# Performance work log

Measured on AMD Instinct MI355X. Metric: run time of the kernel, lower is better.

The kernel has to match this reference:

```python
import jax, jax.numpy as jnp
import numpy as np

BITS = 4
GROUPSIZE = 128
IN_FEATURES = 4096
OUT_FEATURES = 11008
PACK = 32 // BITS  # 8 nibbles per int32
MASK = (1 << BITS) - 1


def setup_inputs() -> dict:
    key = jax.random.key(0)
    k1, k2, k3, k4, k5 = jax.random.split(key, 5)
    x = jax.random.normal(k1, (4, 2048, IN_FEATURES), dtype=jnp.float32)
    qweight = jax.random.randint(k2, (IN_FEATURES // 32 * BITS, OUT_FEATURES), 0, 2147483647, dtype=jnp.int32)
    n_groups = IN_FEATURES // GROUPSIZE  # 32
    qzeros = jax.random.randint(k3, (n_groups, OUT_FEATURES // 32 * BITS), 0, 2147483647, dtype=jnp.int32)
    scales = jax.random.uniform(k4, (n_groups, OUT_FEATURES), dtype=jnp.float32) * 0.01 + 1e-3
    bias = jax.random.normal(k5, (OUT_FEATURES,), dtype=jnp.float32)
    return {"x": x, "qweight": qweight, "qzeros": qzeros, "scales": scales, "bias": bias}


def _dequant(qweight, qzeros, scales):
    # GPTQ 4-bit unpack + group-wise dequant (g_idx=None / non-act-order path).
    shifts = jnp.arange(0, 32, BITS, dtype=jnp.int32)  # [8]
    # zero points: (G, out//8) int32 -> (G, out)
    z = ((qzeros[:, :, None] >> shifts[None, None, :]) & MASK)
    z = z.reshape(qzeros.shape[0], -1).astype(scales.dtype)  # (G, out)
    # weights: (in//8, out) int32 -> (in//8, 8, out) -> (G, groupsize, out)
    w = ((qweight[:, None, :] >> shifts[None, :, None]) & MASK).astype(scales.dtype)
    n_groups = scales.shape[0]
    w = w.reshape(n_groups, GROUPSIZE, -1)
    # W = scale * q - scale * zero, per group
    W = scales[:, None, :] * w - (z * scales)[:, None, :]
    return W.reshape(IN_FEATURES, OUT_FEATURES)


def reference(x, qweight, qzeros, scales, bias):
    W = _dequant(qweight, qzeros, scales)  # (in, out) fp32
    return jnp.matmul(x, W) + bias
```

## Files before the change

### kernel.cpp

```cpp
#include <hip/hip_runtime.h>
#include <hip/hip_bf16.h>
#include <stdint.h>

#define M_DIM 8192
#define K_DIM 4096
#define N_DIM 11008

typedef int i32x4 __attribute__((ext_vector_type(4)));
typedef float f32x4 __attribute__((ext_vector_type(4)));

typedef __attribute__((address_space(1))) const void global_cvoid;
typedef __attribute__((address_space(3))) void lds_void;

__device__ __forceinline__ void gload_lds16(const void* g, void* l) {
  __builtin_amdgcn_global_load_lds((global_cvoid*)g, (lds_void*)l, 16, 0, 0);
}

__global__ void k_quant_x(const float* __restrict__ x, signed char* __restrict__ xq,
                          float* __restrict__ sx) {
  int m = blockIdx.x;
  int tx = threadIdx.x;
  const float4* row = (const float4*)(x + (size_t)m * K_DIM);
  float4 v[4];
  float mx = 0.f;
  #pragma unroll
  for (int i = 0; i < 4; ++i) {
    v[i] = row[tx * 4 + i];
    mx = fmaxf(mx, fmaxf(fmaxf(fabsf(v[i].x), fabsf(v[i].y)),
                         fmaxf(fabsf(v[i].z), fabsf(v[i].w))));
  }
  #pragma unroll
  for (int off = 1; off < 64; off <<= 1)
    mx = fmaxf(mx, __shfl_xor(mx, off));
  __shared__ float wmx[4];
  if ((tx & 63) == 0) wmx[tx >> 6] = mx;
  __syncthreads();
  mx = fmaxf(fmaxf(wmx[0], wmx[1]), fmaxf(wmx[2], wmx[3]));
  mx = fmaxf(mx, 1e-20f);
  float scale = 127.0f / mx;
  if (tx == 0) sx[m] = mx / 127.0f;
  union { signed char c[16]; uint4 u; } p;
  #pragma unroll
  for (int i = 0; i < 4; ++i) {
    p.c[i * 4 + 0] = (signed char)(int)rintf(v[i].x * scale);
    p.c[i * 4 + 1] = (signed char)(int)rintf(v[i].y * scale);
    p.c[i * 4 + 2] = (signed char)(int)rintf(v[i].z * scale);
    p.c[i * 4 + 3] = (signed char)(int)rintf(v[i].w * scale);
  }
  ((uint4*)(xq + (size_t)m * K_DIM))[tx] = p.u;
}

__global__ void k_dequant_w8(const int* __restrict__ qw, const int* __restrict__ qz,
                             signed char* __restrict__ wt) {
  int n = blockIdx.x * blockDim.x + threadIdx.x;
  int k8_0 = blockIdx.y * 8;
  int g = (k8_0 * 8) >> 7;
  int zq = (qz[g * (N_DIM / 8) + (n >> 3)] >> ((n & 7) * 4)) & 15;
  #pragma unroll
  for (int i = 0; i < 8; ++i) {
    int k8 = k8_0 + i;
    int w = qw[(size_t)k8 * N_DIM + n];
    union { signed char c[8]; uint2 u; } r;
    #pragma unroll
    for (int j = 0; j < 8; ++j)
      r.c[j] = (signed char)(((w >> (4 * j)) & 15) - zq);
    *(uint2*)(wt + (size_t)n * K_DIM + (size_t)k8 * 8) = r.u;
  }
}


#define MFMA16(ks) do { \
  __builtin_amdgcn_s_setprio(1); \
  acci[0][0] = __builtin_amdgcn_mfma_i32_16x16x64_i8(af[0], bf[0], acci[0][0], 0, 0, 0); \
  acci[0][1] = __builtin_amdgcn_mfma_i32_16x16x64_i8(af[0], bf[1], acci[0][1], 0, 0, 0); \
  acci[0][2] = __builtin_amdgcn_mfma_i32_16x16x64_i8(af[0], bf[2], acci[0][2], 0, 0, 0); \
  acci[0][3] = __builtin_amdgcn_mfma_i32_16x16x64_i8(af[0], bf[3], acci[0][3], 0, 0, 0); \
  acci[1][0] = __builtin_amdgcn_mfma_i32_16x16x64_i8(af[1], bf[0], acci[1][0], 0, 0, 0); \
  acci[1][1] = __builtin_amdgcn_mfma_i32_16x16x64_i8(af[1], bf[1], acci[1][1], 0, 0, 0); \
  acci[1][2] = __builtin_amdgcn_mfma_i32_16x16x64_i8(af[1], bf[2], acci[1][2], 0, 0, 0); \
  acci[1][3] = __builtin_amdgcn_mfma_i32_16x16x64_i8(af[1], bf[3], acci[1][3], 0, 0, 0); \
  acci[2][0] = __builtin_amdgcn_mfma_i32_16x16x64_i8(af[2], bf[0], acci[2][0], 0, 0, 0); \
  acci[2][1] = __builtin_amdgcn_mfma_i32_16x16x64_i8(af[2], bf[1], acci[2][1], 0, 0, 0); \
  acci[2][2] = __builtin_amdgcn_mfma_i32_16x16x64_i8(af[2], bf[2], acci[2][2], 0, 0, 0); \
  acci[2][3] = __builtin_amdgcn_mfma_i32_16x16x64_i8(af[2], bf[3], acci[2][3], 0, 0, 0); \
  acci[3][0] = __builtin_amdgcn_mfma_i32_16x16x64_i8(af[3], bf[0], acci[3][0], 0, 0, 0); \
  acci[3][1] = __builtin_amdgcn_mfma_i32_16x16x64_i8(af[3], bf[1], acci[3][1], 0, 0, 0); \
  acci[3][2] = __builtin_amdgcn_mfma_i32_16x16x64_i8(af[3], bf[2], acci[3][2], 0, 0, 0); \
  acci[3][3] = __builtin_amdgcn_mfma_i32_16x16x64_i8(af[3], bf[3], acci[3][3], 0, 0, 0); \
  __builtin_amdgcn_s_setprio(0); \
} while (0)

#define LOADF(buf, ks) do { \
  const unsigned char* base_ = sh + (buf) * 32768; \
  af[0] = *(const i32x4*)(const void*)(base_ + (aoff0 ^ ((ks) << 6))); \
  af[1] = *(const i32x4*)(const void*)(base_ + (aoff1 ^ ((ks) << 6))); \
  af[2] = *(const i32x4*)(const void*)(base_ + (aoff2 ^ ((ks) << 6))); \
  af[3] = *(const i32x4*)(const void*)(base_ + (aoff3 ^ ((ks) << 6))); \
  bf[0] = *(const i32x4*)(const void*)(base_ + 16384 + (boff0 ^ ((ks) << 6))); \
  bf[1] = *(const i32x4*)(const void*)(base_ + 16384 + (boff1 ^ ((ks) << 6))); \
  bf[2] = *(const i32x4*)(const void*)(base_ + 16384 + (boff2 ^ ((ks) << 6))); \
  bf[3] = *(const i32x4*)(const void*)(base_ + 16384 + (boff3 ^ ((ks) << 6))); \
} while (0)

#define STAGE_ALL(buf, kt) do { \
  unsigned char* la_ = sh + (buf) * 32768 + w * 4096; \
  unsigned char* lb_ = la_ + 16384; \
  gload_lds16(pA + (kt) * 128, la_); \
  gload_lds16(pA + 8 * (size_t)K_DIM + (kt) * 128, la_ + 1024); \
  gload_lds16(pA + 16 * (size_t)K_DIM + (kt) * 128, la_ + 2048); \
  gload_lds16(pA + 24 * (size_t)K_DIM + (kt) * 128, la_ + 3072); \
  gload_lds16(pB + (kt) * 128, lb_); \
  gload_lds16(pB + 8 * (size_t)K_DIM + (kt) * 128, lb_ + 1024); \
  gload_lds16(pB + 16 * (size_t)K_DIM + (kt) * 128, lb_ + 2048); \
  gload_lds16(pB + 24 * (size_t)K_DIM + (kt) * 128, lb_ + 3072); \
} while (0)

#define WAIT_VM0 asm volatile("s_waitcnt vmcnt(0)" ::: "memory")
#define BAR() do { __builtin_amdgcn_s_barrier(); asm volatile("" ::: "memory"); } while (0)

__global__ __launch_bounds__(256, 2) void k_gemm8(const signed char* __restrict__ xq,
                                                  const signed char* __restrict__ wq,
                                                  const float* __restrict__ sc,
                                                  const float* __restrict__ sx,
                                                  const float* __restrict__ bias,
                                                  float* __restrict__ out) {
  __shared__ __align__(16) unsigned char sh[2 * 32768];

  const int nwg = gridDim.x;
  int bid = blockIdx.x;
  int swz = (bid & 7) * (nwg >> 3) + (bid >> 3);
  const int ntn = N_DIM / 128;
  int mt = swz / ntn;
  int nt = swz % ntn;

  const int tid = threadIdx.x;
  const int w = tid >> 6;
  const int lane = tid & 63;
  const int wm = w >> 1;
  const int wn = w & 1;
  const int fr = lane & 15;
  const int fq = lane >> 4;
  const int r7 = fr & 7;

  const int srow = lane >> 3;
  const int sslot = (lane & 7) ^ srow;
  const size_t goff = (size_t)srow * K_DIM + (size_t)sslot * 16;
  const signed char* pA = xq + (size_t)(mt * 128 + w * 32) * K_DIM + goff;
  const signed char* pB = wq + (size_t)(nt * 128 + w * 32) * K_DIM + goff;

  const int swb = (fq ^ r7) << 4;
  const int aoff0 = (wm * 64 + 0 * 16 + fr) * 128 + swb;
  const int aoff1 = (wm * 64 + 1 * 16 + fr) * 128 + swb;
  const int aoff2 = (wm * 64 + 2 * 16 + fr) * 128 + swb;
  const int aoff3 = (wm * 64 + 3 * 16 + fr) * 128 + swb;
  const int boff0 = (wn * 64 + 0 * 16 + fr) * 128 + swb;
  const int boff1 = (wn * 64 + 1 * 16 + fr) * 128 + swb;
  const int boff2 = (wn * 64 + 2 * 16 + fr) * 128 + swb;
  const int boff3 = (wn * 64 + 3 * 16 + fr) * 128 + swb;

  const int c0 = nt * 128 + wn * 64 + fr;

  i32x4 acci[4][4] = {};
  f32x4 accf[4][4] = {};
  i32x4 af[4], bf[4];

  STAGE_ALL(0, 0);
  WAIT_VM0;
  BAR();

  for (int t = 0; t < 32; ++t) {
    int buf = t & 1;
    if (t < 31) STAGE_ALL(buf ^ 1, t + 1);
    float sg0 = sc[(size_t)t * N_DIM + c0 + 0];
    float sg1 = sc[(size_t)t * N_DIM + c0 + 16];
    float sg2 = sc[(size_t)t * N_DIM + c0 + 32];
    float sg3 = sc[(size_t)t * N_DIM + c0 + 48];
    LOADF(buf, 0);
    MFMA16(0);
    LOADF(buf, 1);
    MFMA16(1);
    #pragma unroll
    for (int mi = 0; mi < 4; ++mi) {
      #pragma unroll
      for (int r = 0; r < 4; ++r) {
        accf[mi][0][r] += sg0 * (float)acci[mi][0][r];
        accf[mi][1][r] += sg1 * (float)acci[mi][1][r];
        accf[mi][2][r] += sg2 * (float)acci[mi][2][r];
        accf[mi][3][r] += sg3 * (float)acci[mi][3][r];
      }
      acci[mi][0] = (i32x4)(0); acci[mi][1] = (i32x4)(0);
      acci[mi][2] = (i32x4)(0); acci[mi][3] = (i32x4)(0);
    }
    WAIT_VM0;
    BAR();
  }

  const int r0 = mt * 128 + wm * 64 + fq * 4;
  #pragma unroll
  for (int mi = 0; mi < 4; ++mi) {
    float sxr[4];
    #pragma unroll
    for (int r = 0; r < 4; ++r) sxr[r] = sx[r0 + mi * 16 + r];
    #pragma unroll
    for (int nj = 0; nj < 4; ++nj) {
      int col = c0 + nj * 16;
      float bv = bias[col];
      size_t base = (size_t)(r0 + mi * 16) * N_DIM + col;
      #pragma unroll
      for (int r = 0; r < 4; ++r)
        out[base + (size_t)r * N_DIM] = sxr[r] * accf[mi][nj][r] + bv;
    }
  }
}

__global__ void k_fallback(const float* __restrict__ x, const int* __restrict__ qw,
                           const int* __restrict__ qz, const float* __restrict__ sc,
                           const float* __restrict__ bias, float* __restrict__ out) {
  int n = blockIdx.x * blockDim.x + threadIdx.x;
  int m = blockIdx.y;
  const float* xr = x + (size_t)m * K_DIM;
  float acc = 0.f;
  for (int g = 0; g < 32; ++g) {
    float s = sc[g * N_DIM + n];
    int zq = (qz[g * (N_DIM / 8) + (n >> 3)] >> ((n & 7) * 4)) & 15;
    float zs = s * (float)zq;
    for (int k8 = g * 16; k8 < g * 16 + 16; ++k8) {
      int w = qw[(size_t)k8 * N_DIM + n];
      #pragma unroll
      for (int j = 0; j < 8; ++j) {
        float wf = s * (float)((w >> (4 * j)) & 15) - zs;
        acc += wf * xr[k8 * 8 + j];
      }
    }
  }
  out[(size_t)m * N_DIM + n] = acc + bias[n];
}

extern "C" void kernel_launch(void* const* d_in, const int* in_sizes, int n_in,
                              void* d_out, int out_size, void* d_ws, size_t ws_size,
                              hipStream_t stream) {
  const float* x  = (const float*)d_in[0];
  const int* qw   = (const int*)d_in[1];
  const int* qz   = (const int*)d_in[2];
  const float* sc = (const float*)d_in[3];
  const float* bias = (const float*)d_in[4];
  float* out = (float*)d_out;

  const size_t xq_bytes = (size_t)M_DIM * K_DIM;
  const size_t sx_bytes = (size_t)M_DIM * sizeof(float);
  const size_t wq_bytes = (size_t)N_DIM * K_DIM;
  const size_t need = xq_bytes + sx_bytes + wq_bytes;

  if (ws_size >= need) {
    signed char* xq = (signed char*)d_ws;
    float* sx = (float*)((char*)d_ws + xq_bytes);
    signed char* wq = (signed char*)((char*)d_ws + xq_bytes + sx_bytes);
    k_quant_x<<<dim3(M_DIM), dim3(256), 0, stream>>>(x, xq, sx);
    k_dequant_w8<<<dim3(N_DIM / 256, 64), dim3(256), 0, stream>>>(qw, qz, wq);
    k_gemm8<<<dim3((M_DIM / 128) * (N_DIM / 128)), dim3(256), 0, stream>>>(xq, wq, sc, sx, bias, out);
  } else {
    k_fallback<<<dim3(N_DIM / 256, M_DIM), dim3(256), 0, stream>>>(x, qw, qz, sc, bias, out);
  }
}
```

Before: 585.0 us.

## Load A fragments directly to registers, stage only B in LDS, merge prep kernels

The GEMM now reads the int8 activation fragments straight from global memory into registers, with a register double-buffer across K tiles, and stages only the weight tile through LDS. This halves LDS usage and LDS reads per tile. The MFMA chain now starts each tile from a zero accumulator, which removes the explicit zeroing. The activation-quantisation and weight-dequant kernels are merged into one launch to save a kernel boundary. The cost is more VGPR pressure and uncoalesced 16-byte global loads for A that no longer go through swizzled LDS.

```diff
diff --git a/kernel.cpp b/kernel.cpp
--- a/kernel.cpp
+++ b/kernel.cpp
@@ -16,107 +16,163 @@
   __builtin_amdgcn_global_load_lds((global_cvoid*)g, (lds_void*)l, 16, 0, 0);
 }
 
-__global__ void k_quant_x(const float* __restrict__ x, signed char* __restrict__ xq,
-                          float* __restrict__ sx) {
-  int m = blockIdx.x;
-  int tx = threadIdx.x;
-  const float4* row = (const float4*)(x + (size_t)m * K_DIM);
-  float4 v[4];
-  float mx = 0.f;
-  #pragma unroll
-  for (int i = 0; i < 4; ++i) {
-    v[i] = row[tx * 4 + i];
-    mx = fmaxf(mx, fmaxf(fmaxf(fabsf(v[i].x), fabsf(v[i].y)),
-                         fmaxf(fabsf(v[i].z), fabsf(v[i].w))));
-  }
-  #pragma unroll
-  for (int off = 1; off < 64; off <<= 1)
-    mx = fmaxf(mx, __shfl_xor(mx, off));
-  __shared__ float wmx[4];
-  if ((tx & 63) == 0) wmx[tx >> 6] = mx;
-  __syncthreads();
-  mx = fmaxf(fmaxf(wmx[0], wmx[1]), fmaxf(wmx[2], wmx[3]));
-  mx = fmaxf(mx, 1e-20f);
-  float scale = 127.0f / mx;
-  if (tx == 0) sx[m] = mx / 127.0f;
-  union { signed char c[16]; uint4 u; } p;
-  #pragma unroll
-  for (int i = 0; i < 4; ++i) {
-    p.c[i * 4 + 0] = (signed char)(int)rintf(v[i].x * scale);
-    p.c[i * 4 + 1] = (signed char)(int)rintf(v[i].y * scale);
-    p.c[i * 4 + 2] = (signed char)(int)rintf(v[i].z * scale);
-    p.c[i * 4 + 3] = (signed char)(int)rintf(v[i].w * scale);
-  }
-  ((uint4*)(xq + (size_t)m * K_DIM))[tx] = p.u;
-}
-
-__global__ void k_dequant_w8(const int* __restrict__ qw, const int* __restrict__ qz,
-                             signed char* __restrict__ wt) {
-  int n = blockIdx.x * blockDim.x + threadIdx.x;
-  int k8_0 = blockIdx.y * 8;
-  int g = (k8_0 * 8) >> 7;
-  int zq = (qz[g * (N_DIM / 8) + (n >> 3)] >> ((n & 7) * 4)) & 15;
-  #pragma unroll
-  for (int i = 0; i < 8; ++i) {
-    int k8 = k8_0 + i;
-    int w = qw[(size_t)k8 * N_DIM + n];
-    union { signed char c[8]; uint2 u; } r;
-    #pragma unroll
-    for (int j = 0; j < 8; ++j)
-      r.c[j] = (signed char)(((w >> (4 * j)) & 15) - zq);
-    *(uint2*)(wt + (size_t)n * K_DIM + (size_t)k8 * 8) = r.u;
-  }
-}
-
-
-#define MFMA16(ks) do { \
+__global__ void k_prep(const float* __restrict__ x, signed char* __restrict__ xq,
+                       float* __restrict__ sx, const int* __restrict__ qw,
+                       const int* __restrict__ qz, signed char* __restrict__ wt) {
+  if (blockIdx.x < M_DIM) {
+    int m = blockIdx.x;
+    int tx = threadIdx.x;
+    const float4* row = (const float4*)(x + (size_t)m * K_DIM);
+    float4 v[4];
+    float mx = 0.f;
+    #pragma unroll
+    for (int i = 0; i < 4; ++i) {
+      v[i] = row[tx * 4 + i];
+      mx = fmaxf(mx, fmaxf(fmaxf(fabsf(v[i].x), fabsf(v[i].y)),
+                           fmaxf(fabsf(v[i].z), fabsf(v[i].w))));
+    }
+    #pragma unroll
+    for (int off = 1; off < 64; off <<= 1)
+      mx = fmaxf(mx, __shfl_xor(mx, off));
+    __shared__ float wmx[4];
+    if ((tx & 63) == 0) wmx[tx >> 6] = mx;
+    __syncthreads();
+    mx = fmaxf(fmaxf(wmx[0], wmx[1]), fmaxf(wmx[2], wmx[3]));
+    mx = fmaxf(mx, 1e-20f);
+    float scale = 127.0f / mx;
+    if (tx == 0) sx[m] = mx / 127.0f;
+    union { signed char c[16]; uint4 u; } p;
+    #pragma unroll
+    for (int i = 0; i < 4; ++i) {
+      p.c[i * 4 + 0] = (signed char)(int)rintf(v[i].x * scale);
+      p.c[i * 4 + 1] = (signed char)(int)rintf(v[i].y * scale);
+      p.c[i * 4 + 2] = (signed char)(int)rintf(v[i].z * scale);
+      p.c[i * 4 + 3] = (signed char)(int)rintf(v[i].w * scale);
+    }
+    ((uint4*)(xq + (size_t)m * K_DIM))[tx] = p.u;
+  } else {
+    int b = blockIdx.x - M_DIM;
+    int n = (b % 43) * 256 + threadIdx.x;
+    int k8_0 = (b / 43) * 8;
+    int g = (k8_0 * 8) >> 7;
+    int zq = (qz[g * (N_DIM / 8) + (n >> 3)] >> ((n & 7) * 4)) & 15;
+    #pragma unroll
+    for (int i = 0; i < 8; ++i) {
+      int k8 = k8_0 + i;
+      int w = qw[(size_t)k8 * N_DIM + n];
+      union { signed char c[8]; uint2 u; } r;
+      #pragma unroll
+      for (int j = 0; j < 8; ++j)
+        r.c[j] = (signed char)(((w >> (4 * j)) & 15) - zq);
+      *(uint2*)(wt + (size_t)n * K_DIM + (size_t)k8 * 8) = r.u;
+    }
+  }
+}
+
+
+#define MFMA_FIRST(S) do { \
   __builtin_amdgcn_s_setprio(1); \
-  acci[0][0] = __builtin_amdgcn_mfma_i32_16x16x64_i8(af[0], bf[0], acci[0][0], 0, 0, 0); \
-  acci[0][1] = __builtin_amdgcn_mfma_i32_16x16x64_i8(af[0], bf[1], acci[0][1], 0, 0, 0); \
-  acci[0][2] = __builtin_amdgcn_mfma_i32_16x16x64_i8(af[0], bf[2], acci[0][2], 0, 0, 0); \
-  acci[0][3] = __builtin_amdgcn_mfma_i32_16x16x64_i8(af[0], bf[3], acci[0][3], 0, 0, 0); \
-  acci[1][0] = __builtin_amdgcn_mfma_i32_16x16x64_i8(af[1], bf[0], acci[1][0], 0, 0, 0); \
-  acci[1][1] = __builtin_amdgcn_mfma_i32_16x16x64_i8(af[1], bf[1], acci[1][1], 0, 0, 0); \
-  acci[1][2] = __builtin_amdgcn_mfma_i32_16x16x64_i8(af[1], bf[2], acci[1][2], 0, 0, 0); \
-  acci[1][3] = __builtin_amdgcn_mfma_i32_16x16x64_i8(af[1], bf[3], acci[1][3], 0, 0, 0); \
-  acci[2][0] = __builtin_amdgcn_mfma_i32_16x16x64_i8(af[2], bf[0], acci[2][0], 0, 0, 0); \
-  acci[2][1] = __builtin_amdgcn_mfma_i32_16x16x64_i8(af[2], bf[1], acci[2][1], 0, 0, 0); \
-  acci[2][2] = __builtin_amdgcn_mfma_i32_16x16x64_i8(af[2], bf[2], acci[2][2], 0, 0, 0); \
-  acci[2][3] = __builtin_amdgcn_mfma_i32_16x16x64_i8(af[2], bf[3], acci[2][3], 0, 0, 0); \
-  acci[3][0] = __builtin_amdgcn_mfma_i32_16x16x64_i8(af[3], bf[0], acci[3][0], 0, 0, 0); \
-  acci[3][1] = __builtin_amdgcn_mfma_i32_16x16x64_i8(af[3], bf[1], acci[3][1], 0, 0, 0); \
-  acci[3][2] = __builtin_amdgcn_mfma_i32_16x16x64_i8(af[3], bf[2], acci[3][2], 0, 0, 0); \
-  acci[3][3] = __builtin_amdgcn_mfma_i32_16x16x64_i8(af[3], bf[3], acci[3][3], 0, 0, 0); \
+  acci[0][0] = __builtin_amdgcn_mfma_i32_16x16x64_i8(S[0][0], bfr[0][0], zq4, 0, 0, 0); \
+  acci[0][1] = __builtin_amdgcn_mfma_i32_16x16x64_i8(S[0][0], bfr[1][0], zq4, 0, 0, 0); \
+  acci[0][2] = __builtin_amdgcn_mfma_i32_16x16x64_i8(S[0][0], bfr[2][0], zq4, 0, 0, 0); \
+  acci[0][3] = __builtin_amdgcn_mfma_i32_16x16x64_i8(S[0][0], bfr[3][0], zq4, 0, 0, 0); \
+  acci[1][0] = __builtin_amdgcn_mfma_i32_16x16x64_i8(S[1][0], bfr[0][0], zq4, 0, 0, 0); \
+  acci[1][1] = __builtin_amdgcn_mfma_i32_16x16x64_i8(S[1][0], bfr[1][0], zq4, 0, 0, 0); \
+  acci[1][2] = __builtin_amdgcn_mfma_i32_16x16x64_i8(S[1][0], bfr[2][0], zq4, 0, 0, 0); \
+  acci[1][3] = __builtin_amdgcn_mfma_i32_16x16x64_i8(S[1][0], bfr[3][0], zq4, 0, 0, 0); \
+  acci[2][0] = __builtin_amdgcn_mfma_i32_16x16x64_i8(S[2][0], bfr[0][0], zq4, 0, 0, 0); \
+  acci[2][1] = __builtin_amdgcn_mfma_i32_16x16x64_i8(S[2][0], bfr[1][0], zq4, 0, 0, 0); \
+  acci[2][2] = __builtin_amdgcn_mfma_i32_16x16x64_i8(S[2][0], bfr[2][0], zq4, 0, 0, 0); \
+  acci[2][3] = __builtin_amdgcn_mfma_i32_16x16x64_i8(S[2][0], bfr[3][0], zq4, 0, 0, 0); \
+  acci[3][0] = __builtin_amdgcn_mfma_i32_16x16x64_i8(S[3][0], bfr[0][0], zq4, 0, 0, 0); \
+  acci[3][1] = __builtin_amdgcn_mfma_i32_16x16x64_i8(S[3][0], bfr[1][0], zq4, 0, 0, 0); \
+  acci[3][2] = __builtin_amdgcn_mfma_i32_16x16x64_i8(S[3][0], bfr[2][0], zq4, 0, 0, 0); \
+  acci[3][3] = __builtin_amdgcn_mfma_i32_16x16x64_i8(S[3][0], bfr[3][0], zq4, 0, 0, 0); \
   __builtin_amdgcn_s_setprio(0); \
 } while (0)
 
-#define LOADF(buf, ks) do { \
-  const unsigned char* base_ = sh + (buf) * 32768; \
-  af[0] = *(const i32x4*)(const void*)(base_ + (aoff0 ^ ((ks) << 6))); \
-  af[1] = *(const i32x4*)(const void*)(base_ + (aoff1 ^ ((ks) << 6))); \
-  af[2] = *(const i32x4*)(const void*)(base_ + (aoff2 ^ ((ks) << 6))); \
-  af[3] = *(const i32x4*)(const void*)(base_ + (aoff3 ^ ((ks) << 6))); \
-  bf[0] = *(const i32x4*)(const void*)(base_ + 16384 + (boff0 ^ ((ks) << 6))); \
-  bf[1] = *(const i32x4*)(const void*)(base_ + 16384 + (boff1 ^ ((ks) << 6))); \
-  bf[2] = *(const i32x4*)(const void*)(base_ + 16384 + (boff2 ^ ((ks) << 6))); \
-  bf[3] = *(const i32x4*)(const void*)(base_ + 16384 + (boff3 ^ ((ks) << 6))); \
-} while (0)
-
-#define STAGE_ALL(buf, kt) do { \
-  unsigned char* la_ = sh + (buf) * 32768 + w * 4096; \
-  unsigned char* lb_ = la_ + 16384; \
-  gload_lds16(pA + (kt) * 128, la_); \
-  gload_lds16(pA + 8 * (size_t)K_DIM + (kt) * 128, la_ + 1024); \
-  gload_lds16(pA + 16 * (size_t)K_DIM + (kt) * 128, la_ + 2048); \
-  gload_lds16(pA + 24 * (size_t)K_DIM + (kt) * 128, la_ + 3072); \
+#define MFMA_SECOND(S) do { \
+  __builtin_amdgcn_s_setprio(1); \
+  acci[0][0] = __builtin_amdgcn_mfma_i32_16x16x64_i8(S[0][1], bfr[0][1], acci[0][0], 0, 0, 0); \
+  acci[0][1] = __builtin_amdgcn_mfma_i32_16x16x64_i8(S[0][1], bfr[1][1], acci[0][1], 0, 0, 0); \
+  acci[0][2] = __builtin_amdgcn_mfma_i32_16x16x64_i8(S[0][1], bfr[2][1], acci[0][2], 0, 0, 0); \
+  acci[0][3] = __builtin_amdgcn_mfma_i32_16x16x64_i8(S[0][1], bfr[3][1], acci[0][3], 0, 0, 0); \
+  acci[1][0] = __builtin_amdgcn_mfma_i32_16x16x64_i8(S[1][1], bfr[0][1], acci[1][0], 0, 0, 0); \
+  acci[1][1] = __builtin_amdgcn_mfma_i32_16x16x64_i8(S[1][1], bfr[1][1], acci[1][1], 0, 0, 0); \
+  acci[1][2] = __builtin_amdgcn_mfma_i32_16x16x64_i8(S[1][1], bfr[2][1], acci[1][2], 0, 0, 0); \
+  acci[1][3] = __builtin_amdgcn_mfma_i32_16x16x64_i8(S[1][1], bfr[3][1], acci[1][3], 0, 0, 0); \
+  acci[2][0] = __builtin_amdgcn_mfma_i32_16x16x64_i8(S[2][1], bfr[0][1], acci[2][0], 0, 0, 0); \
+  acci[2][1] = __builtin_amdgcn_mfma_i32_16x16x64_i8(S[2][1], bfr[1][1], acci[2][1], 0, 0, 0); \
+  acci[2][2] = __builtin_amdgcn_mfma_i32_16x16x64_i8(S[2][1], bfr[2][1], acci[2][2], 0, 0, 0); \
+  acci[2][3] = __builtin_amdgcn_mfma_i32_16x16x64_i8(S[2][1], bfr[3][1], acci[2][3], 0, 0, 0); \
+  acci[3][0] = __builtin_amdgcn_mfma_i32_16x16x64_i8(S[3][1], bfr[0][1], acci[3][0], 0, 0, 0); \
+  acci[3][1] = __builtin_amdgcn_mfma_i32_16x16x64_i8(S[3][1], bfr[1][1], acci[3][1], 0, 0, 0); \
+  acci[3][2] = __builtin_amdgcn_mfma_i32_16x16x64_i8(S[3][1], bfr[2][1], acci[3][2], 0, 0, 0); \
+  acci[3][3] = __builtin_amdgcn_mfma_i32_16x16x64_i8(S[3][1], bfr[3][1], acci[3][3], 0, 0, 0); \
+  __builtin_amdgcn_s_setprio(0); \
+} while (0)
+
+#define AFETCH(S, kt) do { \
+  const signed char* a_ = pAg + (size_t)(kt) * 128; \
+  S[0][0] = *(const i32x4*)(const void*)(a_); \
+  S[0][1] = *(const i32x4*)(const void*)(a_ + 64); \
+  S[1][0] = *(const i32x4*)(const void*)(a_ + 16 * (size_t)K_DIM); \
+  S[1][1] = *(const i32x4*)(const void*)(a_ + 16 * (size_t)K_DIM + 64); \
+  S[2][0] = *(const i32x4*)(const void*)(a_ + 32 * (size_t)K_DIM); \
+  S[2][1] = *(const i32x4*)(const void*)(a_ + 32 * (size_t)K_DIM + 64); \
+  S[3][0] = *(const i32x4*)(const void*)(a_ + 48 * (size_t)K_DIM); \
+  S[3][1] = *(const i32x4*)(const void*)(a_ + 48 * (size_t)K_DIM + 64); \
+} while (0)
+
+#define LOADBF(buf) do { \
+  const unsigned char* b_ = sh + (buf) * 16384; \
+  bfr[0][0] = *(const i32x4*)(const void*)(b_ + (boff0)); \
+  bfr[0][1] = *(const i32x4*)(const void*)(b_ + (boff0 ^ 64)); \
+  bfr[1][0] = *(const i32x4*)(const void*)(b_ + (boff1)); \
+  bfr[1][1] = *(const i32x4*)(const void*)(b_ + (boff1 ^ 64)); \
+  bfr[2][0] = *(const i32x4*)(const void*)(b_ + (boff2)); \
+  bfr[2][1] = *(const i32x4*)(const void*)(b_ + (boff2 ^ 64)); \
+  bfr[3][0] = *(const i32x4*)(const void*)(b_ + (boff3)); \
+  bfr[3][1] = *(const i32x4*)(const void*)(b_ + (boff3 ^ 64)); \
+} while (0)
+
+#define STAGE_B(buf, kt) do { \
+  unsigned char* lb_ = sh + (buf) * 16384 + w * 4096; \
   gload_lds16(pB + (kt) * 128, lb_); \
   gload_lds16(pB + 8 * (size_t)K_DIM + (kt) * 128, lb_ + 1024); \
   gload_lds16(pB + 16 * (size_t)K_DIM + (kt) * 128, lb_ + 2048); \
   gload_lds16(pB + 24 * (size_t)K_DIM + (kt) * 128, lb_ + 3072); \
 } while (0)
 
+#define FOLD(t) do { \
+  float sg0 = sc[(size_t)(t) * N_DIM + c0 + 0]; \
+  float sg1 = sc[(size_t)(t) * N_DIM + c0 + 16]; \
+  float sg2 = sc[(size_t)(t) * N_DIM + c0 + 32]; \
+  float sg3 = sc[(size_t)(t) * N_DIM + c0 + 48]; \
+  _Pragma("unroll") \
+  for (int mi = 0; mi < 4; ++mi) { \
+    _Pragma("unroll") \
+    for (int r = 0; r < 4; ++r) { \
+      accf[mi][0][r] += sg0 * (float)acci[mi][0][r]; \
+      accf[mi][1][r] += sg1 * (float)acci[mi][1][r]; \
+      accf[mi][2][r] += sg2 * (float)acci[mi][2][r]; \
+      accf[mi][3][r] += sg3 * (float)acci[mi][3][r]; \
+    } \
+  } \
+} while (0)
+
 #define WAIT_VM0 asm volatile("s_waitcnt vmcnt(0)" ::: "memory")
 #define BAR() do { __builtin_amdgcn_s_barrier(); asm volatile("" ::: "memory"); } while (0)
+
+#define TILE(Scur, Snxt, buf, t, LASTP) do { \
+  if (!(LASTP)) { AFETCH(Snxt, (t) + 1); STAGE_B((buf) ^ 1, (t) + 1); } \
+  LOADBF(buf); \
+  MFMA_FIRST(Scur); \
+  MFMA_SECOND(Scur); \
+  FOLD(t); \
+  WAIT_VM0; \
+  BAR(); \
+} while (0)
 
 __global__ __launch_bounds__(256, 2) void k_gemm8(const signed char* __restrict__ xq,
                                                   const signed char* __restrict__ wq,
@@ -124,7 +180,7 @@
                                                   const float* __restrict__ sx,
                                                   const float* __restrict__ bias,
                                                   float* __restrict__ out) {
-  __shared__ __align__(16) unsigned char sh[2 * 32768];
+  __shared__ __align__(16) unsigned char sh[2 * 16384];
 
   const int nwg = gridDim.x;
   int bid = blockIdx.x;
@@ -142,17 +198,13 @@
   const int fq = lane >> 4;
   const int r7 = fr & 7;
 
+  const signed char* pAg = xq + (size_t)(mt * 128 + wm * 64 + fr) * K_DIM + fq * 16;
+
   const int srow = lane >> 3;
   const int sslot = (lane & 7) ^ srow;
-  const size_t goff = (size_t)srow * K_DIM + (size_t)sslot * 16;
-  const signed char* pA = xq + (size_t)(mt * 128 + w * 32) * K_DIM + goff;
-  const signed char* pB = wq + (size_t)(nt * 128 + w * 32) * K_DIM + goff;
+  const signed char* pB = wq + (size_t)(nt * 128 + w * 32 + srow) * K_DIM + (size_t)sslot * 16;
 
   const int swb = (fq ^ r7) << 4;
-  const int aoff0 = (wm * 64 + 0 * 16 + fr) * 128 + swb;
-  const int aoff1 = (wm * 64 + 1 * 16 + fr) * 128 + swb;
-  const int aoff2 = (wm * 64 + 2 * 16 + fr) * 128 + swb;
-  const int aoff3 = (wm * 64 + 3 * 16 + fr) * 128 + swb;
   const int boff0 = (wn * 64 + 0 * 16 + fr) * 128 + swb;
   const int boff1 = (wn * 64 + 1 * 16 + fr) * 128 + swb;
   const int boff2 = (wn * 64 + 2 * 16 + fr) * 128 + swb;
@@ -160,39 +212,21 @@
 
   const int c0 = nt * 128 + wn * 64 + fr;
 
-  i32x4 acci[4][4] = {};
+  i32x4 acci[4][4];
   f32x4 accf[4][4] = {};
-  i32x4 af[4], bf[4];
-
-  STAGE_ALL(0, 0);
+  i32x4 afA[4][2], afB[4][2];
+  i32x4 bfr[4][2];
+  const i32x4 zq4 = {0, 0, 0, 0};
+
+  AFETCH(afA, 0);
+  STAGE_B(0, 0);
   WAIT_VM0;
   BAR();
 
-  for (int t = 0; t < 32; ++t) {
-    int buf = t & 1;
-    if (t < 31) STAGE_ALL(buf ^ 1, t + 1);
-    float sg0 = sc[(size_t)t * N_DIM + c0 + 0];
-    float sg1 = sc[(size_t)t * N_DIM + c0 + 16];
-    float sg2 = sc[(size_t)t * N_DIM + c0 + 32];
-    float sg3 = sc[(size_t)t * N_DIM + c0 + 48];
-    LOADF(buf, 0);
-    MFMA16(0);
-    LOADF(buf, 1);
-    MFMA16(1);
-    #pragma unroll
-    for (int mi = 0; mi < 4; ++mi) {
-      #pragma unroll
-      for (int r = 0; r < 4; ++r) {
-        accf[mi][0][r] += sg0 * (float)acci[mi][0][r];
-        accf[mi][1][r] += sg1 * (float)acci[mi][1][r];
-        accf[mi][2][r] += sg2 * (float)acci[mi][2][r];
-        accf[mi][3][r] += sg3 * (float)acci[mi][3][r];
-      }
-      acci[mi][0] = (i32x4)(0); acci[mi][1] = (i32x4)(0);
-      acci[mi][2] = (i32x4)(0); acci[mi][3] = (i32x4)(0);
-    }
-    WAIT_VM0;
-    BAR();
+  for (int i = 0; i < 16; ++i) {
+    int T0 = 2 * i;
+    TILE(afA, afB, 0, T0, false);
+    TILE(afB, afA, 1, T0 + 1, i == 15);
   }
 
   const int r0 = mt * 128 + wm * 64 + fq * 4;
@@ -255,8 +289,7 @@
     signed char* xq = (signed char*)d_ws;
     float* sx = (float*)((char*)d_ws + xq_bytes);
     signed char* wq = (signed char*)((char*)d_ws + xq_bytes + sx_bytes);
-    k_quant_x<<<dim3(M_DIM), dim3(256), 0, stream>>>(x, xq, sx);
-    k_dequant_w8<<<dim3(N_DIM / 256, 64), dim3(256), 0, stream>>>(qw, qz, wq);
+    k_prep<<<dim3(M_DIM + 2752), dim3(256), 0, stream>>>(x, xq, sx, qw, qz, wq);
     k_gemm8<<<dim3((M_DIM / 128) * (N_DIM / 128)), dim3(256), 0, stream>>>(xq, wq, sc, sx, bias, out);
   } else {
     k_fallback<<<dim3(N_DIM / 256, M_DIM), dim3(256), 0, stream>>>(x, qw, qz, sc, bias, out);
```

Result: slower. 2.095 ms (+258.1%).
